# Performance work log

Measured on AMD Instinct MI355X. Metric: run time of the kernel, lower is better.

The kernel has to match this reference:

```python
import jax, jax.numpy as jnp
import numpy as np

B, T, H, NH = 2, 2048, 1024, 16
HD = H // NH


def setup_inputs() -> dict:
    key = jax.random.key(0)
    ks = jax.random.split(key, 12)
    s = 1.0 / np.sqrt(H)
    inp = {
        "q": jax.random.normal(ks[0], (B, T, H), jnp.float32),
        "k": jax.random.normal(ks[1], (B, T, H), jnp.float32),
        "v": jax.random.normal(ks[2], (B, T, H), jnp.float32),
        "mask": jnp.tril(jnp.ones((T, T), jnp.int32))[None, None],  # causal [1,1,T,T]
        "w_q": jax.random.normal(ks[3], (H, H), jnp.float32) * s,
        "b_q": jax.random.normal(ks[4], (H,), jnp.float32) * 0.01,
        "w_k": jax.random.normal(ks[5], (H, H), jnp.float32) * s,
        "b_k": jax.random.normal(ks[6], (H,), jnp.float32) * 0.01,
        "w_v": jax.random.normal(ks[7], (H, H), jnp.float32) * s,
        "b_v": jax.random.normal(ks[8], (H,), jnp.float32) * 0.01,
        "w_o": jax.random.normal(ks[9], (H, H), jnp.float32) * s,
        "b_o": jax.random.normal(ks[10], (H,), jnp.float32) * 0.01,
    }
    return inp


def reference(q, k, v, mask, w_q, b_q, w_k, b_k, w_v, b_v, w_o, b_o):
    def split_heads(x):
        Bx, Tx, _ = x.shape
        return x.reshape(Bx, Tx, NH, HD).transpose(0, 2, 1, 3)  # [B,NH,T,HD]

    Q = split_heads(q @ w_q.T + b_q)
    K = split_heads(k @ w_k.T + b_k)
    V = split_heads(v @ w_v.T + b_v)

    scores = jnp.einsum("bhqd,bhkd->bhqk", Q, K) / np.sqrt(HD).astype(np.float32)
    scores = jnp.where(mask == 0, jnp.float32(-1e9), scores)
    weights = jax.nn.softmax(scores, axis=-1)  # dropout prob = 0.0
    out = jnp.einsum("bhqk,bhkd->bhqd", weights, V)
    out = out.transpose(0, 2, 1, 3).reshape(q.shape[0], q.shape[1], H)
    return out @ w_o.T + b_o
```

## Files before the change

### kernel.cpp

```cpp
#include <hip/hip_runtime.h>
#include <hip/hip_bf16.h>

#define Bb 2
#define Tt 2048
#define Hh 1024
#define NHh 16

typedef short bf16x8 __attribute__((ext_vector_type(8)));
typedef float f32x4 __attribute__((ext_vector_type(4)));
typedef unsigned short u16;
typedef unsigned int u32;
typedef u16 u16x4v __attribute__((ext_vector_type(4)));
typedef u32 u32x2v __attribute__((ext_vector_type(2)));

#define QK_SCALE 0.180336880f

#if __has_builtin(__builtin_amdgcn_exp2f)
__device__ __forceinline__ float exp2_fast(float x) { return __builtin_amdgcn_exp2f(x); }
#else
__device__ __forceinline__ float exp2_fast(float x) { return __expf(x * 0.69314718f); }
#endif

__device__ __forceinline__ u16 f2b(float x) {
  unsigned u = __builtin_bit_cast(unsigned, x);
  u += 0x7FFFu + ((u >> 16) & 1u);
  return (u16)(u >> 16);
}

__device__ __forceinline__ u32 cvt_pk(float lo, float hi) {
  u32 r;
  asm("v_cvt_pk_bf16_f32 %0, %1, %2" : "=v"(r) : "v"(lo), "v"(hi));
  return r;
}

__global__ __launch_bounds__(256) void cvt3_kernel(const float* __restrict__ s0,
                                                   const float* __restrict__ s1,
                                                   const float* __restrict__ s2,
                                                   u16* __restrict__ d0,
                                                   u16* __restrict__ d1,
                                                   u16* __restrict__ d2, int n4) {
  const int which = blockIdx.y;
  const float* src = which == 0 ? s0 : which == 1 ? s1 : s2;
  u16* dst = which == 0 ? d0 : which == 1 ? d1 : d2;
  int i = blockIdx.x * blockDim.x + threadIdx.x;
  int stride = gridDim.x * blockDim.x;
  for (; i < n4; i += stride) {
    float4 v = ((const float4*)src)[i];
    u16x4v o;
    o.x = f2b(v.x); o.y = f2b(v.y); o.z = f2b(v.z); o.w = f2b(v.w);
    ((u16x4v*)dst)[i] = o;
  }
}

__global__ __launch_bounds__(256) void cvt4_kernel(const float* __restrict__ s0,
                                                   const float* __restrict__ s1,
                                                   const float* __restrict__ s2,
                                                   const float* __restrict__ s3,
                                                   u16* __restrict__ d0,
                                                   u16* __restrict__ d1,
                                                   u16* __restrict__ d2,
                                                   u16* __restrict__ d3, int n4) {
  const int which = blockIdx.y;
  const float* src = which == 0 ? s0 : which == 1 ? s1 : which == 2 ? s2 : s3;
  u16* dst = which == 0 ? d0 : which == 1 ? d1 : which == 2 ? d2 : d3;
  const float sc = (which == 0) ? QK_SCALE : 1.0f;
  int i = blockIdx.x * blockDim.x + threadIdx.x;
  int stride = gridDim.x * blockDim.x;
  for (; i < n4; i += stride) {
    float4 v = ((const float4*)src)[i];
    u16x4v o;
    o.x = f2b(v.x * sc); o.y = f2b(v.y * sc); o.z = f2b(v.z * sc); o.w = f2b(v.w * sc);
    ((u16x4v*)dst)[i] = o;
  }
}

template<int NF, int MODE>
__device__ __forceinline__ void gemm_body(const u16* __restrict__ A,
                                          const u16* __restrict__ W,
                                          const float* __restrict__ bias, float bscale,
                                          void* __restrict__ Cout,
                                          u16* lA, u16* lB, int mt, int nt) {
  const int tid = threadIdx.x;
  const int lane = tid & 63;
  const int wid = tid >> 6;
  const int wr = wid >> 1, wc = wid & 1;
  const int g = lane >> 4, fr = lane & 15;
  constexpr int NT = NF * 32;

  f32x4 acc[4][NF];
#pragma unroll
  for (int m = 0; m < 4; ++m)
#pragma unroll
    for (int n = 0; n < NF; ++n) acc[m][n] = (f32x4){0.f, 0.f, 0.f, 0.f};

  const int srow = tid >> 3;
  const int scol = (tid & 7) * 8;

  bf16x8 ra[4], rb[NF];
#pragma unroll
  for (int ps = 0; ps < 4; ++ps)
    ra[ps] = *(const bf16x8*)(A + (size_t)(mt * 128 + ps * 32 + srow) * Hh + scol);
#pragma unroll
  for (int ps = 0; ps < NF; ++ps)
    rb[ps] = *(const bf16x8*)(W + (size_t)(nt * NT + ps * 32 + srow) * Hh + scol);
#pragma unroll
  for (int ps = 0; ps < 4; ++ps) {
    int r = ps * 32 + srow;
    *(bf16x8*)((char*)lA + r * 128 + ((scol * 2) ^ ((r & 7) << 4))) = ra[ps];
  }
#pragma unroll
  for (int ps = 0; ps < NF; ++ps) {
    int r = ps * 32 + srow;
    *(bf16x8*)((char*)lB + r * 128 + ((scol * 2) ^ ((r & 7) << 4))) = rb[ps];
  }
  __syncthreads();

  for (int kt = 0; kt < Hh; kt += 64) {
    if (kt + 64 < Hh) {
#pragma unroll
      for (int ps = 0; ps < 4; ++ps)
        ra[ps] = *(const bf16x8*)(A + (size_t)(mt * 128 + ps * 32 + srow) * Hh + kt + 64 + scol);
#pragma unroll
      for (int ps = 0; ps < NF; ++ps)
        rb[ps] = *(const bf16x8*)(W + (size_t)(nt * NT + ps * 32 + srow) * Hh + kt + 64 + scol);
    }
    bf16x8 af[4][2], bfv[NF][2];
#pragma unroll
    for (int m = 0; m < 4; ++m)
#pragma unroll
      for (int ks = 0; ks < 2; ++ks) {
        int r = wr * 64 + m * 16 + fr;
        af[m][ks] = *(const bf16x8*)((const char*)lA + r * 128 + ((ks * 64 + g * 16) ^ ((r & 7) << 4)));
      }
#pragma unroll
    for (int n = 0; n < NF; ++n)
#pragma unroll
      for (int ks = 0; ks < 2; ++ks) {
        int r = wc * (NT / 2) + n * 16 + fr;
        bfv[n][ks] = *(const bf16x8*)((const char*)lB + r * 128 + ((ks * 64 + g * 16) ^ ((r & 7) << 4)));
      }
#pragma unroll
    for (int m = 0; m < 4; ++m)
#pragma unroll
      for (int n = 0; n < NF; ++n)
#pragma unroll
        for (int ks = 0; ks < 2; ++ks)
          acc[m][n] = __builtin_amdgcn_mfma_f32_16x16x32_bf16(af[m][ks], bfv[n][ks],
                                                              acc[m][n], 0, 0, 0);
    if (kt + 64 < Hh) {
      __syncthreads();
#pragma unroll
      for (int ps = 0; ps < 4; ++ps) {
        int r = ps * 32 + srow;
        *(bf16x8*)((char*)lA + r * 128 + ((scol * 2) ^ ((r & 7) << 4))) = ra[ps];
      }
#pragma unroll
      for (int ps = 0; ps < NF; ++ps) {
        int r = ps * 32 + srow;
        *(bf16x8*)((char*)lB + r * 128 + ((scol * 2) ^ ((r & 7) << 4))) = rb[ps];
      }
      __syncthreads();
    }
  }

#pragma unroll
  for (int n = 0; n < NF; ++n) {
    int Cc = nt * NT + wc * (NT / 2) + n * 16 + fr;
    float bv = bias[Cc] * bscale;
#pragma unroll
    for (int m = 0; m < 4; ++m) {
#pragma unroll
      for (int j = 0; j < 4; ++j) {
        int R = mt * 128 + wr * 64 + m * 16 + g * 4 + j;
        float val = acc[m][n][j] + bv;
        if constexpr (MODE == 0) {
          int bb = R >> 11, t = R & (Tt - 1);
          int h = Cc >> 6, d = Cc & 63;
          ((u16*)Cout)[(((size_t)(bb * NHh + h) * Tt + t) << 6) + d] = f2b(val);
        } else if constexpr (MODE == 2) {
          int bb = R >> 11, t = R & (Tt - 1);
          int h = Cc >> 6, d = Cc & 63;
          ((u16*)Cout)[(((size_t)(bb * NHh + h) * 64 + d) << 11) + t] = f2b(val);
        } else {
          ((float*)Cout)[(size_t)R * Hh + Cc] = val;
        }
      }
    }
  }
}

__global__ __launch_bounds__(256, 3) void proj_qkv_kernel(
    const u16* __restrict__ qb, const u16* __restrict__ kb, const u16* __restrict__ vb,
    const u16* __restrict__ wqb, const u16* __restrict__ wkb, const u16* __restrict__ wvb,
    const float* __restrict__ biq, const float* __restrict__ bik, const float* __restrict__ biv,
    u16* __restrict__ Qp, u16* __restrict__ Kp, u16* __restrict__ Vt) {
  __shared__ u16 lA[128 * 64];
  __shared__ u16 lB[64 * 64];
  const int id = blockIdx.x;
  const int j = id >> 3;
  const int slot = (id & 7) + 8 * (j >> 4);
  const int nt = j & 15;
  const int z = slot >> 5, mt = slot & 31;
  if (z == 0)      gemm_body<2, 0>(qb, wqb, biq, QK_SCALE, Qp, lA, lB, mt, nt);
  else if (z == 1) gemm_body<2, 0>(kb, wkb, bik, 1.0f, Kp, lA, lB, mt, nt);
  else             gemm_body<2, 2>(vb, wvb, biv, 1.0f, Vt, lA, lB, mt, nt);
}

__global__ __launch_bounds__(256, 2) void gemm_out_kernel(
    const u16* __restrict__ A, const u16* __restrict__ W,
    const float* __restrict__ bias, float* __restrict__ Cout) {
  __shared__ u16 lA[128 * 64];
  __shared__ u16 lB[64 * 64];
  const int id = blockIdx.x;
  const int j = id >> 3;
  const int mt = (id & 7) + 8 * (j >> 4);
  const int nt = j & 15;
  gemm_body<2, 1>(A, W, bias, 1.0f, Cout, lA, lB, mt, nt);
}

__global__ __launch_bounds__(256, 4) void attn_kernel(const u16* __restrict__ Qp,
                                                      const u16* __restrict__ Kp,
                                                      const u16* __restrict__ Vt,
                                                      u16* __restrict__ AO) {
  __shared__ u16 lK[2][64 * 64];
  __shared__ u16 lV[2][64 * 64];
  __shared__ u16 lP[64 * 64];
  const int tid = threadIdx.x;
  const int lane = tid & 63;
  const int w = tid >> 6;
  const int g = lane >> 4, fr = lane & 15;
  const int L = blockIdx.x;
  const int i = L & 255, k4 = L >> 8;
  const int bh = i & 31, s8 = i >> 5;
  const int t2 = s8 * 2 + (k4 >> 1);
  const int qt = (k4 & 1) ? (31 - t2) : t2;
  const int q0 = qt * 64;

  bf16x8 qf[2];
  {
    const u16* qrow = Qp + (((size_t)bh * Tt + q0 + w * 16 + fr) << 6) + g * 8;
    qf[0] = *(const bf16x8*)(qrow);
    qf[1] = *(const bf16x8*)(qrow + 32);
  }

  const int srow = tid >> 3;
  const int scol = (tid & 7) * 8;
  const int sswz = (scol * 2) ^ ((srow & 7) << 4);

  bf16x8 rk[2], rv[2];
#pragma unroll
  for (int ps = 0; ps < 2; ++ps) {
    rk[ps] = *(const bf16x8*)(Kp + (((size_t)bh * Tt + ps * 32 + srow) << 6) + scol);
    rv[ps] = *(const bf16x8*)(Vt + (((size_t)bh * 64 + ps * 32 + srow) << 11) + scol);
  }
#pragma unroll
  for (int ps = 0; ps < 2; ++ps) {
    *(bf16x8*)((char*)lK[0] + (ps * 32 + srow) * 128 + sswz) = rk[ps];
    *(bf16x8*)((char*)lV[0] + (ps * 32 + srow) * 128 + sswz) = rv[ps];
  }
  __syncthreads();

  float m_r = -1e30f, l_r = 0.f;
  f32x4 acc[4];
#pragma unroll
  for (int nd = 0; nd < 4; ++nd) acc[nd] = (f32x4){0.f, 0.f, 0.f, 0.f};

  const int prow = w * 16 + fr;
  const int psw = (prow & 7) << 4;
  const int qoff = w * 16 + fr;

  for (int jt = 0; jt <= qt; ++jt) {
    const char* bK = (const char*)lK[jt & 1];
    const char* bV = (const char*)lV[jt & 1];
    if (jt < qt) {
#pragma unroll
      for (int ps = 0; ps < 2; ++ps) {
        rk[ps] = *(const bf16x8*)(Kp + (((size_t)bh * Tt + (jt + 1) * 64 + ps * 32 + srow) << 6) + scol);
        rv[ps] = *(const bf16x8*)(Vt + (((size_t)bh * 64 + ps * 32 + srow) << 11) + (jt + 1) * 64 + scol);
      }
    }
    f32x4 s[4];
    __builtin_amdgcn_s_setprio(1);
#pragma unroll
    for (int n = 0; n < 4; ++n) {
      s[n] = (f32x4){0.f, 0.f, 0.f, 0.f};
      int rbase = (n * 16 + fr) * 128;
      int rsw = (fr & 7) << 4;
#pragma unroll
      for (int ks = 0; ks < 2; ++ks) {
        bf16x8 ak = *(const bf16x8*)(bK + rbase + ((ks * 64 + g * 16) ^ rsw));
        s[n] = __builtin_amdgcn_mfma_f32_16x16x32_bf16(ak, qf[ks], s[n], 0, 0, 0);
      }
    }
    __builtin_amdgcn_s_setprio(0);

    float tm = -1e30f;
    if (jt == qt) {
#pragma unroll
      for (int n = 0; n < 4; ++n)
#pragma unroll
        for (int r = 0; r < 4; ++r) {
          if (n * 16 + g * 4 + r > qoff) s[n][r] = -1e30f;
          tm = fmaxf(tm, s[n][r]);
        }
    } else {
#pragma unroll
      for (int n = 0; n < 4; ++n)
#pragma unroll
        for (int r = 0; r < 4; ++r) tm = fmaxf(tm, s[n][r]);
    }
    tm = fmaxf(tm, __shfl_xor(tm, 16));
    tm = fmaxf(tm, __shfl_xor(tm, 32));
    if (!__all(tm <= m_r + 8.0f)) {
      float mn = fmaxf(m_r, tm);
      float sc = exp2_fast(m_r - mn);
      m_r = mn;
      l_r *= sc;
      float scj[4];
#pragma unroll
      for (int j = 0; j < 4; ++j) scj[j] = __shfl(sc, g * 4 + j);
#pragma unroll
      for (int nd = 0; nd < 4; ++nd)
#pragma unroll
        for (int j = 0; j < 4; ++j) acc[nd][j] *= scj[j];
    }
    float rs = 0.f;
    u32 pw[4][2];
#pragma unroll
    for (int n = 0; n < 4; ++n) {
      float p0 = exp2_fast(s[n][0] - m_r);
      float p1 = exp2_fast(s[n][1] - m_r);
      float p2 = exp2_fast(s[n][2] - m_r);
      float p3 = exp2_fast(s[n][3] - m_r);
      rs += (p0 + p1) + (p2 + p3);
      pw[n][0] = cvt_pk(p0, p1);
      pw[n][1] = cvt_pk(p2, p3);
    }
    rs += __shfl_xor(rs, 16);
    rs += __shfl_xor(rs, 32);
    l_r += rs;
    bf16x8 pa[2];
    {
      char* base = (char*)lP + prow * 128;
#pragma unroll
      for (int n = 0; n < 4; ++n)
        *(u32x2v*)(base + ((32 * n + 8 * g) ^ psw)) = (u32x2v){pw[n][0], pw[n][1]};
#pragma unroll
      for (int ks = 0; ks < 2; ++ks)
        pa[ks] = *(const bf16x8*)(base + ((ks * 64 + g * 16) ^ psw));
    }
    __builtin_amdgcn_s_setprio(1);
#pragma unroll
    for (int nd = 0; nd < 4; ++nd) {
      int rbase = (nd * 16 + fr) * 128;
      int rsw = (fr & 7) << 4;
#pragma unroll
      for (int ks = 0; ks < 2; ++ks) {
        bf16x8 bv = *(const bf16x8*)(bV + rbase + ((ks * 64 + g * 16) ^ rsw));
        acc[nd] = __builtin_amdgcn_mfma_f32_16x16x32_bf16(pa[ks], bv, acc[nd], 0, 0, 0);
      }
    }
    __builtin_amdgcn_s_setprio(0);
    if (jt < qt) {
#pragma unroll
      for (int ps = 0; ps < 2; ++ps) {
        *(bf16x8*)((char*)lK[(jt + 1) & 1] + (ps * 32 + srow) * 128 + sswz) = rk[ps];
        *(bf16x8*)((char*)lV[(jt + 1) & 1] + (ps * 32 + srow) * 128 + sswz) = rv[ps];
      }
      __syncthreads();
    }
  }

  const int b = bh >> 4, hh = bh & 15;
  float lj[4];
#pragma unroll
  for (int j = 0; j < 4; ++j) lj[j] = __shfl(l_r, g * 4 + j);
#pragma unroll
  for (int j = 0; j < 4; ++j) {
    float inv = 1.0f / lj[j];
    int qq = q0 + w * 16 + g * 4 + j;
    size_t base = (((size_t)b * Tt + qq) << 10) + hh * 64;
#pragma unroll
    for (int nd = 0; nd < 4; ++nd)
      AO[base + nd * 16 + fr] = f2b(acc[nd][j] * inv);
  }
}

extern "C" void kernel_launch(void* const* d_in, const int* in_sizes, int n_in,
                              void* d_out, int out_size, void* d_ws, size_t ws_size,
                              hipStream_t stream) {
  const float* q   = (const float*)d_in[0];
  const float* k   = (const float*)d_in[1];
  const float* v   = (const float*)d_in[2];
  const float* wq  = (const float*)d_in[4];
  const float* bq  = (const float*)d_in[5];
  const float* wk  = (const float*)d_in[6];
  const float* bk  = (const float*)d_in[7];
  const float* wv  = (const float*)d_in[8];
  const float* bv  = (const float*)d_in[9];
  const float* wo  = (const float*)d_in[10];
  const float* bo  = (const float*)d_in[11];

  char* ws = (char*)d_ws;
  const size_t SZB = (size_t)Bb * Tt * Hh * 2;
  const size_t WB  = (size_t)Hh * Hh * 2;
  u16* qb  = (u16*)(ws);
  u16* kb  = (u16*)(ws + SZB);
  u16* vb  = (u16*)(ws + 2 * SZB);
  u16* wqb = (u16*)(ws + 3 * SZB);
  u16* wkb = (u16*)(ws + 3 * SZB + WB);
  u16* wvb = (u16*)(ws + 3 * SZB + 2 * WB);
  u16* wob = (u16*)(ws + 3 * SZB + 3 * WB);
  u16* Qp  = (u16*)(ws + 3 * SZB + 4 * WB);
  u16* Kp  = (u16*)(ws + 4 * SZB + 4 * WB);
  u16* Vt  = (u16*)(ws + 5 * SZB + 4 * WB);
  u16* AO  = qb;

  const int N4_IN = (Bb * Tt * Hh) / 4;
  const int N4_W  = (Hh * Hh) / 4;
  cvt3_kernel<<<dim3(512, 3), 256, 0, stream>>>(q, k, v, qb, kb, vb, N4_IN);
  cvt4_kernel<<<dim3(128, 4), 256, 0, stream>>>(wq, wk, wv, wo, wqb, wkb, wvb, wob, N4_W);

  proj_qkv_kernel<<<dim3(1536), 256, 0, stream>>>(
      qb, kb, vb, wqb, wkb, wvb, bq, bk, bv, Qp, Kp, Vt);

  attn_kernel<<<dim3(1024), 256, 0, stream>>>(Qp, Kp, Vt, AO);

  gemm_out_kernel<<<dim3(512), 256, 0, stream>>>(
      AO, wob, bo, (float*)d_out);
}
```

Before: 114.4 us.

## Merge conversion kernels, single-buffer attention LDS, raise occupancy bounds

The two fp32-to-bf16 conversion launches become one seven-way kernel, removing a launch. Attention drops its double-buffered K/V shared memory to a single buffer with an extra barrier before each refill, so more blocks fit per CU, and its launch bound rises to 6. The projection GEMM launch bound also rises from 3 to 4. The risks are that the added barrier serializes the LDS refill with compute, and that the tighter register budgets may cause spills.

New measurement: 126.3 us. +10.3%, slower.

```diff
diff --git a/kernel.cpp b/kernel.cpp
--- a/kernel.cpp
+++ b/kernel.cpp
@@ -33,43 +33,33 @@
   return r;
 }
 
-__global__ __launch_bounds__(256) void cvt3_kernel(const float* __restrict__ s0,
-                                                   const float* __restrict__ s1,
-                                                   const float* __restrict__ s2,
-                                                   u16* __restrict__ d0,
-                                                   u16* __restrict__ d1,
-                                                   u16* __restrict__ d2, int n4) {
+__global__ __launch_bounds__(256) void cvt_all_kernel(
+    const float* __restrict__ q, const float* __restrict__ k, const float* __restrict__ v,
+    const float* __restrict__ wq, const float* __restrict__ wk,
+    const float* __restrict__ wv, const float* __restrict__ wo,
+    u16* __restrict__ qb, u16* __restrict__ kb, u16* __restrict__ vb,
+    u16* __restrict__ wqb, u16* __restrict__ wkb, u16* __restrict__ wvb,
+    u16* __restrict__ wob, int n4_in, int n4_w) {
   const int which = blockIdx.y;
-  const float* src = which == 0 ? s0 : which == 1 ? s1 : s2;
-  u16* dst = which == 0 ? d0 : which == 1 ? d1 : d2;
+  const float* src;
+  u16* dst;
+  int n4;
+  float sc = 1.0f;
+  switch (which) {
+    case 0: src = q;  dst = qb;  n4 = n4_in; break;
+    case 1: src = k;  dst = kb;  n4 = n4_in; break;
+    case 2: src = v;  dst = vb;  n4 = n4_in; break;
+    case 3: src = wq; dst = wqb; n4 = n4_w; sc = QK_SCALE; break;
+    case 4: src = wk; dst = wkb; n4 = n4_w; break;
+    case 5: src = wv; dst = wvb; n4 = n4_w; break;
+    default: src = wo; dst = wob; n4 = n4_w; break;
+  }
   int i = blockIdx.x * blockDim.x + threadIdx.x;
   int stride = gridDim.x * blockDim.x;
   for (; i < n4; i += stride) {
-    float4 v = ((const float4*)src)[i];
+    float4 vv = ((const float4*)src)[i];
     u16x4v o;
-    o.x = f2b(v.x); o.y = f2b(v.y); o.z = f2b(v.z); o.w = f2b(v.w);
-    ((u16x4v*)dst)[i] = o;
-  }
-}
-
-__global__ __launch_bounds__(256) void cvt4_kernel(const float* __restrict__ s0,
-                                                   const float* __restrict__ s1,
-                                                   const float* __restrict__ s2,
-                                                   const float* __restrict__ s3,
-                                                   u16* __restrict__ d0,
-                                                   u16* __restrict__ d1,
-                                                   u16* __restrict__ d2,
-                                                   u16* __restrict__ d3, int n4) {
-  const int which = blockIdx.y;
-  const float* src = which == 0 ? s0 : which == 1 ? s1 : which == 2 ? s2 : s3;
-  u16* dst = which == 0 ? d0 : which == 1 ? d1 : which == 2 ? d2 : d3;
-  const float sc = (which == 0) ? QK_SCALE : 1.0f;
-  int i = blockIdx.x * blockDim.x + threadIdx.x;
-  int stride = gridDim.x * blockDim.x;
-  for (; i < n4; i += stride) {
-    float4 v = ((const float4*)src)[i];
-    u16x4v o;
-    o.x = f2b(v.x * sc); o.y = f2b(v.y * sc); o.z = f2b(v.z * sc); o.w = f2b(v.w * sc);
+    o.x = f2b(vv.x * sc); o.y = f2b(vv.y * sc); o.z = f2b(vv.z * sc); o.w = f2b(vv.w * sc);
     ((u16x4v*)dst)[i] = o;
   }
 }
@@ -189,7 +179,7 @@
   }
 }
 
-__global__ __launch_bounds__(256, 3) void proj_qkv_kernel(
+__global__ __launch_bounds__(256, 4) void proj_qkv_kernel(
     const u16* __restrict__ qb, const u16* __restrict__ kb, const u16* __restrict__ vb,
     const u16* __restrict__ wqb, const u16* __restrict__ wkb, const u16* __restrict__ wvb,
     const float* __restrict__ biq, const float* __restrict__ bik, const float* __restrict__ biv,
@@ -218,12 +208,12 @@
   gemm_body<2, 1>(A, W, bias, 1.0f, Cout, lA, lB, mt, nt);
 }
 
-__global__ __launch_bounds__(256, 4) void attn_kernel(const u16* __restrict__ Qp,
+__global__ __launch_bounds__(256, 6) void attn_kernel(const u16* __restrict__ Qp,
                                                       const u16* __restrict__ Kp,
                                                       const u16* __restrict__ Vt,
                                                       u16* __restrict__ AO) {
-  __shared__ u16 lK[2][64 * 64];
-  __shared__ u16 lV[2][64 * 64];
+  __shared__ u16 lK[64 * 64];
+  __shared__ u16 lV[64 * 64];
   __shared__ u16 lP[64 * 64];
   const int tid = threadIdx.x;
   const int lane = tid & 63;
@@ -255,8 +245,8 @@
   }
 #pragma unroll
   for (int ps = 0; ps < 2; ++ps) {
-    *(bf16x8*)((char*)lK[0] + (ps * 32 + srow) * 128 + sswz) = rk[ps];
-    *(bf16x8*)((char*)lV[0] + (ps * 32 + srow) * 128 + sswz) = rv[ps];
+    *(bf16x8*)((char*)lK + (ps * 32 + srow) * 128 + sswz) = rk[ps];
+    *(bf16x8*)((char*)lV + (ps * 32 + srow) * 128 + sswz) = rv[ps];
   }
   __syncthreads();
 
@@ -270,8 +260,6 @@
   const int qoff = w * 16 + fr;
 
   for (int jt = 0; jt <= qt; ++jt) {
-    const char* bK = (const char*)lK[jt & 1];
-    const char* bV = (const char*)lV[jt & 1];
     if (jt < qt) {
 #pragma unroll
       for (int ps = 0; ps < 2; ++ps) {
@@ -288,7 +276,7 @@
       int rsw = (fr & 7) << 4;
 #pragma unroll
       for (int ks = 0; ks < 2; ++ks) {
-        bf16x8 ak = *(const bf16x8*)(bK + rbase + ((ks * 64 + g * 16) ^ rsw));
+        bf16x8 ak = *(const bf16x8*)((const char*)lK + rbase + ((ks * 64 + g * 16) ^ rsw));
         s[n] = __builtin_amdgcn_mfma_f32_16x16x32_bf16(ak, qf[ks], s[n], 0, 0, 0);
       }
     }
@@ -356,16 +344,17 @@
       int rsw = (fr & 7) << 4;
 #pragma unroll
       for (int ks = 0; ks < 2; ++ks) {
-        bf16x8 bv = *(const bf16x8*)(bV + rbase + ((ks * 64 + g * 16) ^ rsw));
+        bf16x8 bv = *(const bf16x8*)((const char*)lV + rbase + ((ks * 64 + g * 16) ^ rsw));
         acc[nd] = __builtin_amdgcn_mfma_f32_16x16x32_bf16(pa[ks], bv, acc[nd], 0, 0, 0);
       }
     }
     __builtin_amdgcn_s_setprio(0);
     if (jt < qt) {
+      __syncthreads();
 #pragma unroll
       for (int ps = 0; ps < 2; ++ps) {
-        *(bf16x8*)((char*)lK[(jt + 1) & 1] + (ps * 32 + srow) * 128 + sswz) = rk[ps];
-        *(bf16x8*)((char*)lV[(jt + 1) & 1] + (ps * 32 + srow) * 128 + sswz) = rv[ps];
+        *(bf16x8*)((char*)lK + (ps * 32 + srow) * 128 + sswz) = rk[ps];
+        *(bf16x8*)((char*)lV + (ps * 32 + srow) * 128 + sswz) = rv[ps];
       }
       __syncthreads();
     }
@@ -418,8 +407,8 @@
 
   const int N4_IN = (Bb * Tt * Hh) / 4;
   const int N4_W  = (Hh * Hh) / 4;
-  cvt3_kernel<<<dim3(512, 3), 256, 0, stream>>>(q, k, v, qb, kb, vb, N4_IN);
-  cvt4_kernel<<<dim3(128, 4), 256, 0, stream>>>(wq, wk, wv, wo, wqb, wkb, wvb, wob, N4_W);
+  cvt_all_kernel<<<dim3(512, 7), 256, 0, stream>>>(
+      q, k, v, wq, wk, wv, wo, qb, kb, vb, wqb, wkb, wvb, wob, N4_IN, N4_W);
 
   proj_qkv_kernel<<<dim3(1536), 256, 0, stream>>>(
       qb, kb, vb, wqb, wkb, wvb, bq, bk, bv, Qp, Kp, Vt);
```
